# Performance work log

Hardware: AMD Instinct MI355X
Metric: run time of the kernel (lower is better)

Reference implementation:

```python
import jax, jax.numpy as jnp
import numpy as np

N_NODES = 100000
N_EDGES = 3200000
D_FEAT = 128
HIDDEN = 64
N_GRAPHS = 64


def gcn_conv(x, W, b, src, dst, deg_inv_sqrt):
    # PyG GCNConv: h = D^-1/2 (A+I) D^-1/2 (x @ W) + b, with self-loops.
    h = x @ W  # [N, out]
    coeff = deg_inv_sqrt[src] * deg_inv_sqrt[dst]  # [E]
    agg = jax.ops.segment_sum(coeff[:, None] * h[src], dst, num_segments=N_NODES)
    # self-loop contribution: deg^-1 * h
    agg = agg + (deg_inv_sqrt * deg_inv_sqrt)[:, None] * h
    return agg + b


def setup_inputs() -> dict:
    key = jax.random.key(0)
    ks = jax.random.split(key, 16)
    x = jax.random.normal(ks[0], (N_NODES, D_FEAT), dtype=jnp.float32)
    edge_index = jax.random.randint(ks[1], (2, N_EDGES), 0, N_NODES, dtype=jnp.int64)
    batch = jnp.sort(jax.random.randint(ks[2], (N_NODES,), 0, N_GRAPHS, dtype=jnp.int64))
    sc_in = 1.0 / np.sqrt(D_FEAT)
    sc_h = 1.0 / np.sqrt(HIDDEN)
    return {
        "x": x,
        "edge_index": edge_index,
        "batch": batch,
        "W1": jax.random.uniform(ks[3], (D_FEAT, HIDDEN), jnp.float32, -sc_in, sc_in),
        "b1": jnp.zeros((HIDDEN,), jnp.float32),
        "mlpW": jax.random.uniform(ks[4], (HIDDEN, HIDDEN), jnp.float32, -sc_h, sc_h),
        "mlpb": jax.random.uniform(ks[5], (HIDDEN,), jnp.float32, -sc_h, sc_h),
        "W2": jax.random.uniform(ks[6], (HIDDEN, HIDDEN), jnp.float32, -sc_h, sc_h),
        "b2": jnp.zeros((HIDDEN,), jnp.float32),
        "W3": jax.random.uniform(ks[7], (HIDDEN, HIDDEN), jnp.float32, -sc_h, sc_h),
        "b3": jnp.zeros((HIDDEN,), jnp.float32),
        "linW": jax.random.uniform(ks[8], (HIDDEN, 1), jnp.float32, -sc_h, sc_h),
        "linb": jax.random.uniform(ks[9], (1,), jnp.float32, -sc_h, sc_h),
    }


def reference(x, edge_index, batch, W1, b1, mlpW, mlpb, W2, b2, W3, b3, linW, linb):
    src, dst = edge_index[0], edge_index[1]
    # symmetric gcn_norm degrees (with self-loop), computed once from dst
    deg = jax.ops.segment_sum(jnp.ones((N_EDGES,), x.dtype), dst, num_segments=N_NODES) + 1.0
    deg_inv_sqrt = jax.lax.rsqrt(deg)

    h = jax.nn.relu(gcn_conv(x, W1, b1, src, dst, deg_inv_sqrt))
    h = jax.nn.relu(h @ mlpW + mlpb)  # mlp1 (Linear); edge_index arg in source is a no-op
    h = jax.nn.relu(gcn_conv(h, W2, b2, src, dst, deg_inv_sqrt))
    h = jax.nn.relu(gcn_conv(h, W3, b3, src, dst, deg_inv_sqrt))

    # global_mean_pool over graphs
    sums = jax.ops.segment_sum(h, batch, num_segments=N_GRAPHS)  # [G, H]
    counts = jax.ops.segment_sum(jnp.ones((N_NODES,), h.dtype), batch, num_segments=N_GRAPHS)
    pooled = sums / jnp.maximum(counts, 1.0)[:, None]

    # dropout p=0.5 is identity in eval mode
    return pooled @ linW + linb  # [G, 1]
```

## Files before the change

### kernel.cpp

```cpp
#include <hip/hip_runtime.h>

#define NN 100000
#define NE 3200000
#define DF 128
#define NH 64
#define NG 64

#define BKN 256
#define NB2 ((NN + BKN - 1) / BKN)
#define CAP2 8832
#define PART_E 8192
#define PART_T 512
#define PART_NBLK ((NE + PART_E - 1) / PART_E)
#define ELLW 64

typedef _Float16 h16;
typedef unsigned char f8;
typedef __fp16 hv2 __attribute__((ext_vector_type(2)));
typedef __fp16 hv4 __attribute__((ext_vector_type(4)));
typedef float fv4 __attribute__((ext_vector_type(4)));

#define FSCALE 16.0f
#define INV_FSCALE 0.0625f

__device__ __forceinline__ f8 to_f8(float v) {
    int pk = __builtin_amdgcn_cvt_pk_fp8_f32(v, v, 0, false);
    return (f8)(pk & 0xFF);
}

__device__ __forceinline__ float dot2h(unsigned a, unsigned b, float c) {
    return __builtin_amdgcn_fdot2(__builtin_bit_cast(hv2, a),
                                  __builtin_bit_cast(hv2, b), c, false);
}

__device__ __forceinline__ unsigned pack_pair(float v) {
    int nb = __builtin_amdgcn_mov_dpp(__builtin_bit_cast(int, v), 0xB1, 0xF, 0xF, true);
    return __builtin_bit_cast(unsigned,
        __builtin_amdgcn_cvt_pkrtz(v, __builtin_bit_cast(float, nb)));
}

__device__ __forceinline__ unsigned pack_rtn(float a, float b) {
    unsigned ua = (unsigned)__builtin_bit_cast(unsigned short, (h16)a);
    unsigned ub = (unsigned)__builtin_bit_cast(unsigned short, (h16)b);
    return ua | (ub << 16);
}


__global__ void k_init(int* __restrict__ bcur) {
    int i = threadIdx.x;
    if (i < NB2) bcur[i] = i * CAP2;
}


__global__ __launch_bounds__(PART_T) void k_part(const int* __restrict__ src,
                                                 const int* __restrict__ dst,
                                                 int* __restrict__ bcur,
                                                 int* __restrict__ tmp) {
    __shared__ int ds[PART_E];
    __shared__ int hist[NB2];
    __shared__ int base[NB2];
    int t = threadIdx.x;
    int e0 = blockIdx.x * PART_E;
    int ne = NE - e0; if (ne > PART_E) ne = PART_E;

    for (int b = t; b < NB2; b += PART_T) hist[b] = 0;
    __syncthreads();
    for (int i = t; i < ne; i += PART_T) {
        int d = dst[e0 + i];
        ds[i] = d;
        atomicAdd(&hist[d >> 8], 1);
    }
    __syncthreads();
    for (int b = t; b < NB2; b += PART_T)
        base[b] = atomicAdd(&bcur[b], hist[b]);
    __syncthreads();
    for (int i = t; i < ne; i += PART_T) {
        int d = ds[i];
        int s = src[e0 + i];
        int pos = atomicAdd(&base[d >> 8], 1);
        tmp[pos] = (s << 8) | (d & (BKN - 1));
    }
}


__global__ __launch_bounds__(256) void k_build(const int* __restrict__ bcur,
                                               const int* __restrict__ tmp,
                                               float* __restrict__ dis,
                                               int* __restrict__ cnt,
                                               int* __restrict__ csr,
                                               float* __restrict__ sums,
                                               f8* __restrict__ A,
                                               f8* __restrict__ B) {
    __shared__ int h[BKN];
    __shared__ int cur[BKN];
    int b = blockIdx.x, t = threadIdx.x;
    if (b == 0) { for (int i = t; i < NG * NH + NG; i += 256) sums[i] = 0.f; }
    if (b == 1 && t < NH) {
        A[(size_t)NN * NH + t] = 0;
        B[(size_t)NN * NH + t] = 0;
    }
    h[t] = 0;
    __syncthreads();
    int beg = b * CAP2, end = bcur[b];
    for (int i = beg + t; i < end; i += 256) atomicAdd(&h[tmp[i] & (BKN - 1)], 1);
    __syncthreads();
    int node = b * BKN + t;
    int real = h[t];
    int rmax = h[t & ~1] > h[t | 1] ? h[t & ~1] : h[t | 1];
    int common = (rmax + 3) & ~3;
    if (node < NN) {
        dis[node] = rsqrtf((float)real + 1.0f);
        cnt[node] = common;
    }
    cur[t] = 0;
    __syncthreads();
    for (int i = beg + t; i < end; i += 256) {
        int e = tmp[i];
        int d = e & (BKN - 1);
        int j = atomicAdd(&cur[d], 1);
        int nd = b * BKN + d;
        int pos = ((nd >> 1) << 7) + ((j >> 2) << 3) + ((nd & 1) << 2) + (j & 3);
        csr[pos] = (e >> 8) << 6;
    }
    __syncthreads();
    if (node < NN) {
        int pbase = (node >> 1) << 7;
        int half = (node & 1) << 2;
        for (int j = real; j < common; j++)
            csr[pbase + ((j >> 2) << 3) + half + (j & 3)] = NN << 6;
    }
}


__global__ __launch_bounds__(256) void k_gemm1(const float* __restrict__ x,
                                               const float* __restrict__ W1,
                                               const float* __restrict__ dis,
                                               f8* __restrict__ out) {
    int t = threadIdx.x;
    int lane = t & 63;
    int tile = blockIdx.x * 4 + (t >> 6);
    if (tile >= NN / 16) return;
    int r16 = lane & 15, g4 = lane >> 4;

    hv4 b[4][8];
#pragma unroll
    for (int s = 0; s < 8; s++) {
#pragma unroll
        for (int ct = 0; ct < 4; ct++) {
            const float* wp = W1 + (s * 16 + g4 * 4) * NH + ct * 16 + r16;
            hv4 bb;
            bb[0] = (h16)wp[0];
            bb[1] = (h16)wp[NH];
            bb[2] = (h16)wp[2 * NH];
            bb[3] = (h16)wp[3 * NH];
            b[ct][s] = bb;
        }
    }

    int nb = tile * 16;
    const float* xw = x + (size_t)(nb + r16) * DF + g4 * 4;
    fv4 xr[8];
#pragma unroll
    for (int s = 0; s < 8; s++) xr[s] = *(const fv4*)(xw + s * 16);

    fv4 acc[4] = {fv4{0.f, 0.f, 0.f, 0.f}, fv4{0.f, 0.f, 0.f, 0.f},
                  fv4{0.f, 0.f, 0.f, 0.f}, fv4{0.f, 0.f, 0.f, 0.f}};
#pragma unroll
    for (int s = 0; s < 8; s++) {
        hv4 a;
        a[0] = (h16)xr[s][0]; a[1] = (h16)xr[s][1];
        a[2] = (h16)xr[s][2]; a[3] = (h16)xr[s][3];
#pragma unroll
        for (int ct = 0; ct < 4; ct++)
            acc[ct] = __builtin_amdgcn_mfma_f32_16x16x16f16(a, b[ct][s], acc[ct], 0, 0, 0);
    }

    float dv[4];
#pragma unroll
    for (int r = 0; r < 4; r++) dv[r] = dis[nb + g4 * 4 + r] * FSCALE;
#pragma unroll
    for (int ct = 0; ct < 4; ct++) {
#pragma unroll
        for (int r = 0; r < 4; r++) {
            int n = nb + g4 * 4 + r;
            out[((unsigned)n << 6) | (unsigned)(ct * 16 + r16)] = to_f8(dv[r] * acc[ct][r]);
        }
    }
}


__device__ __forceinline__ float f8_ld(const f8* __restrict__ hs, unsigned off) {
    return __builtin_amdgcn_cvt_f32_fp8((int)hs[off], 0);
}

#define ACC8(qa, qb)                                                    \
    do {                                                                \
        a0 += f8_ld(hs, ((unsigned)(qa).x) | lane);                     \
        a1 += f8_ld(hs, ((unsigned)(qa).y) | lane);                     \
        a0 += f8_ld(hs, ((unsigned)(qa).z) | lane);                     \
        a1 += f8_ld(hs, ((unsigned)(qa).w) | lane);                     \
        b0 += f8_ld(hs, ((unsigned)(qb).x) | lane);                     \
        b1 += f8_ld(hs, ((unsigned)(qb).y) | lane);                     \
        b0 += f8_ld(hs, ((unsigned)(qb).z) | lane);                     \
        b1 += f8_ld(hs, ((unsigned)(qb).w) | lane);                     \
    } while (0)

__device__ __forceinline__ void gather_pair(const int* __restrict__ csr,
                                            const int* __restrict__ cnt,
                                            const f8* __restrict__ hs,
                                            int p, unsigned lane,
                                            float& g0, float& g1) {
    int beg = __builtin_amdgcn_readfirstlane(p << 7);
    int len = __builtin_amdgcn_readfirstlane(cnt[2 * p]);
    int end = beg + 2 * len;
    float a0 = f8_ld(hs, ((unsigned)(2 * p) << 6) | lane);
    float b0 = f8_ld(hs, ((unsigned)(2 * p + 1) << 6) | lane);
    float a1 = 0.f, b1 = 0.f;
    int k = beg;
    if (k + 16 <= end) {
        int4 qa = *(const int4*)(csr + k);
        int4 qb = *(const int4*)(csr + k + 4);
        int4 qc = *(const int4*)(csr + k + 8);
        int4 qd = *(const int4*)(csr + k + 12);
        for (; k + 32 <= end; k += 16) {
            int4 na = *(const int4*)(csr + k + 16);
            int4 nb = *(const int4*)(csr + k + 20);
            int4 nc = *(const int4*)(csr + k + 24);
            int4 nd = *(const int4*)(csr + k + 28);
            ACC8(qa, qb);
            ACC8(qc, qd);
            qa = na; qb = nb; qc = nc; qd = nd;
        }
        ACC8(qa, qb);
        ACC8(qc, qd);
        k += 16;
    }
    if (k + 8 <= end) {
        int4 qa = *(const int4*)(csr + k);
        int4 qb = *(const int4*)(csr + k + 4);
        ACC8(qa, qb);
    }
    g0 = a0 + a1;
    g1 = b0 + b1;
}


__global__ __launch_bounds__(1024) void k_gather_mm2(const int* __restrict__ cnt,
                                                     const int* __restrict__ csr,
                                                     const float* __restrict__ dis,
                                                     const f8* __restrict__ hs,
                                                     const float* __restrict__ bin,
                                                     const float* __restrict__ W1m,
                                                     const float* __restrict__ bmid,
                                                     const float* __restrict__ W2m,
                                                     f8* __restrict__ outp) {
    __shared__ unsigned w1p[(NH / 2) * NH];
    __shared__ unsigned w2p[(NH / 2) * NH];
    __shared__ unsigned pvl[16][2][NH / 2];
    __shared__ float b_in[NH], b_mid[NH];
    int t = threadIdx.x;
    for (int i = t; i < (NH / 2) * NH; i += 1024) {
        int k2 = i >> 6, o = i & 63;
        w1p[i] = pack_rtn(W1m[(2 * k2) * NH + o], W1m[(2 * k2 + 1) * NH + o]);
        w2p[i] = pack_rtn(W2m[(2 * k2) * NH + o], W2m[(2 * k2 + 1) * NH + o]);
    }
    if (t < NH) { b_in[t] = bin[t]; b_mid[t] = bmid[t]; }
    __syncthreads();

    int wave = t >> 6, lane = t & 63;
    int p = blockIdx.x * 16 + wave;
    int n0 = 2 * p, n1 = 2 * p + 1;
    float d0 = dis[n0], d1 = dis[n1];

    float g0, g1;
    gather_pair(csr, cnt, hs, p, (unsigned)lane, g0, g1);
    float v0 = fmaxf(g0 * (d0 * INV_FSCALE) + b_in[lane], 0.f);
    float v1 = fmaxf(g1 * (d1 * INV_FSCALE) + b_in[lane], 0.f);

    unsigned pv0 = pack_pair(v0), pv1 = pack_pair(v1);
    if (!(lane & 1)) {
        pvl[wave][0][lane >> 1] = pv0;
        pvl[wave][1][lane >> 1] = pv1;
    }
    float m0 = 0.f, m1 = 0.f;
#pragma unroll
    for (int k4 = 0; k4 < 8; k4++) {
        int4 a0 = *(const int4*)&pvl[wave][0][k4 * 4];
        int4 a1 = *(const int4*)&pvl[wave][1][k4 * 4];
        unsigned wv;
        wv = w1p[(k4 * 4 + 0) * NH + lane]; m0 = dot2h((unsigned)a0.x, wv, m0); m1 = dot2h((unsigned)a1.x, wv, m1);
        wv = w1p[(k4 * 4 + 1) * NH + lane]; m0 = dot2h((unsigned)a0.y, wv, m0); m1 = dot2h((unsigned)a1.y, wv, m1);
        wv = w1p[(k4 * 4 + 2) * NH + lane]; m0 = dot2h((unsigned)a0.z, wv, m0); m1 = dot2h((unsigned)a1.z, wv, m1);
        wv = w1p[(k4 * 4 + 3) * NH + lane]; m0 = dot2h((unsigned)a0.w, wv, m0); m1 = dot2h((unsigned)a1.w, wv, m1);
    }
    m0 = fmaxf(m0 + b_mid[lane], 0.f);
    m1 = fmaxf(m1 + b_mid[lane], 0.f);

    unsigned pm0 = pack_pair(m0), pm1 = pack_pair(m1);
    if (!(lane & 1)) {
        pvl[wave][0][lane >> 1] = pm0;
        pvl[wave][1][lane >> 1] = pm1;
    }
    float o0 = 0.f, o1 = 0.f;
#pragma unroll
    for (int k4 = 0; k4 < 8; k4++) {
        int4 a0 = *(const int4*)&pvl[wave][0][k4 * 4];
        int4 a1 = *(const int4*)&pvl[wave][1][k4 * 4];
        unsigned wv;
        wv = w2p[(k4 * 4 + 0) * NH + lane]; o0 = dot2h((unsigned)a0.x, wv, o0); o1 = dot2h((unsigned)a1.x, wv, o1);
        wv = w2p[(k4 * 4 + 1) * NH + lane]; o0 = dot2h((unsigned)a0.y, wv, o0); o1 = dot2h((unsigned)a1.y, wv, o1);
        wv = w2p[(k4 * 4 + 2) * NH + lane]; o0 = dot2h((unsigned)a0.z, wv, o0); o1 = dot2h((unsigned)a1.z, wv, o1);
        wv = w2p[(k4 * 4 + 3) * NH + lane]; o0 = dot2h((unsigned)a0.w, wv, o0); o1 = dot2h((unsigned)a1.w, wv, o1);
    }
    outp[((unsigned)n0 << 6) | (unsigned)lane] = to_f8(d0 * o0 * FSCALE);
    outp[((unsigned)n1 << 6) | (unsigned)lane] = to_f8(d1 * o1 * FSCALE);
}


__global__ __launch_bounds__(1024) void k_gather_mm1(const int* __restrict__ cnt,
                                                     const int* __restrict__ csr,
                                                     const float* __restrict__ dis,
                                                     const f8* __restrict__ hs,
                                                     const float* __restrict__ bin,
                                                     const float* __restrict__ W1m,
                                                     f8* __restrict__ outp) {
    __shared__ unsigned w1p[(NH / 2) * NH];
    __shared__ unsigned pvl[16][2][NH / 2];
    __shared__ float b_in[NH];
    int t = threadIdx.x;
    for (int i = t; i < (NH / 2) * NH; i += 1024) {
        int k2 = i >> 6, o = i & 63;
        w1p[i] = pack_rtn(W1m[(2 * k2) * NH + o], W1m[(2 * k2 + 1) * NH + o]);
    }
    if (t < NH) b_in[t] = bin[t];
    __syncthreads();

    int wave = t >> 6, lane = t & 63;
    int p = blockIdx.x * 16 + wave;
    int n0 = 2 * p, n1 = 2 * p + 1;
    float d0 = dis[n0], d1 = dis[n1];

    float g0, g1;
    gather_pair(csr, cnt, hs, p, (unsigned)lane, g0, g1);
    float v0 = fmaxf(g0 * (d0 * INV_FSCALE) + b_in[lane], 0.f);
    float v1 = fmaxf(g1 * (d1 * INV_FSCALE) + b_in[lane], 0.f);

    unsigned pv0 = pack_pair(v0), pv1 = pack_pair(v1);
    if (!(lane & 1)) {
        pvl[wave][0][lane >> 1] = pv0;
        pvl[wave][1][lane >> 1] = pv1;
    }
    float o0 = 0.f, o1 = 0.f;
#pragma unroll
    for (int k4 = 0; k4 < 8; k4++) {
        int4 a0 = *(const int4*)&pvl[wave][0][k4 * 4];
        int4 a1 = *(const int4*)&pvl[wave][1][k4 * 4];
        unsigned wv;
        wv = w1p[(k4 * 4 + 0) * NH + lane]; o0 = dot2h((unsigned)a0.x, wv, o0); o1 = dot2h((unsigned)a1.x, wv, o1);
        wv = w1p[(k4 * 4 + 1) * NH + lane]; o0 = dot2h((unsigned)a0.y, wv, o0); o1 = dot2h((unsigned)a1.y, wv, o1);
        wv = w1p[(k4 * 4 + 2) * NH + lane]; o0 = dot2h((unsigned)a0.z, wv, o0); o1 = dot2h((unsigned)a1.z, wv, o1);
        wv = w1p[(k4 * 4 + 3) * NH + lane]; o0 = dot2h((unsigned)a0.w, wv, o0); o1 = dot2h((unsigned)a1.w, wv, o1);
    }
    outp[((unsigned)n0 << 6) | (unsigned)lane] = to_f8(d0 * o0 * FSCALE);
    outp[((unsigned)n1 << 6) | (unsigned)lane] = to_f8(d1 * o1 * FSCALE);
}


__global__ __launch_bounds__(1024) void k_gather_pool(const int* __restrict__ cnt,
                                                      const int* __restrict__ csr,
                                                      const float* __restrict__ dis,
                                                      const f8* __restrict__ hs,
                                                      const float* __restrict__ b3,
                                                      const int* __restrict__ batch,
                                                      float* __restrict__ sums,
                                                      float* __restrict__ cntf) {
    __shared__ float rows[32][NH];
    __shared__ int gids[32];
    int t = threadIdx.x;
    int wave = t >> 6, lane = t & 63;
    int p = blockIdx.x * 16 + wave;
    int n0 = 2 * p, n1 = 2 * p + 1;
    {
        float d0 = dis[n0], d1 = dis[n1];
        float g0, g1;
        gather_pair(csr, cnt, hs, p, (unsigned)lane, g0, g1);
        rows[2 * wave][lane]     = fmaxf(g0 * (d0 * INV_FSCALE) + b3[lane], 0.f);
        rows[2 * wave + 1][lane] = fmaxf(g1 * (d1 * INV_FSCALE) + b3[lane], 0.f);
        if (lane == 0) { gids[2 * wave] = batch[n0]; gids[2 * wave + 1] = batch[n1]; }
    }
    __syncthreads();
    if (wave == 0) {
        float acc = 0.f; float cl = 0.f;
        int cur = gids[0];
        for (int i = 0; i < 32; i++) {
            int g = gids[i];
            if (g != cur) {
                atomicAdd(&sums[cur * NH + lane], acc);
                if (lane == 0) atomicAdd(&cntf[cur], cl);
                acc = 0.f; cl = 0.f; cur = g;
            }
            acc += rows[i][lane];
            cl += 1.f;
        }
        atomicAdd(&sums[cur * NH + lane], acc);
        if (lane == 0) atomicAdd(&cntf[cur], cl);
    }
}


__global__ void k_final(const float* __restrict__ sums, const float* __restrict__ cnt,
                        const float* __restrict__ linW, const float* __restrict__ linb,
                        float* __restrict__ out) {
    int g = blockIdx.x;
    int lane = threadIdx.x;
    float v = sums[g * NH + lane] * linW[lane];
#pragma unroll
    for (int off = 32; off > 0; off >>= 1) v += __shfl_down(v, off);
    if (lane == 0) out[g] = v / fmaxf(cnt[g], 1.f) + linb[0];
}


extern "C" void kernel_launch(void* const* d_in, const int* in_sizes, int n_in,
                              void* d_out, int out_size, void* d_ws, size_t ws_size,
                              hipStream_t stream) {
    const float* x    = (const float*)d_in[0];
    const int*   ei   = (const int*)d_in[1];
    const int*   batch= (const int*)d_in[2];
    const float* W1   = (const float*)d_in[3];
    const float* b1   = (const float*)d_in[4];
    const float* mlpW = (const float*)d_in[5];
    const float* mlpb = (const float*)d_in[6];
    const float* W2   = (const float*)d_in[7];
    const float* b2   = (const float*)d_in[8];
    const float* W3   = (const float*)d_in[9];
    const float* b3   = (const float*)d_in[10];
    const float* linW = (const float*)d_in[11];
    const float* linb = (const float*)d_in[12];
    float* out = (float*)d_out;

    char* p = (char*)d_ws;
    int*   csr  = (int*)p;                p += (size_t)NN * ELLW * 4;
    f8*    A    = (f8*)p;                 p += (size_t)(NN + 1) * NH;
    f8*    B    = (f8*)p;                 p += (size_t)(NN + 1) * NH;
    int*   tmp  = (int*)p;                p += (size_t)NB2 * CAP2 * 4;
    float* dis  = (float*)p;              p += NN * 4;
    float* sums = (float*)p;              p += NG * NH * 4;
    float* cntf = (float*)p;              p += NG * 4;
    int*   cnt  = (int*)p;                p += NN * 4;
    int*   bcur = (int*)p;                p += 512 * 4;

    const int* src = ei;
    const int* dst = ei + NE;

    k_init<<<1, 512, 0, stream>>>(bcur);
    k_part<<<PART_NBLK, PART_T, 0, stream>>>(src, dst, bcur, tmp);
    k_build<<<NB2, 256, 0, stream>>>(bcur, tmp, dis, cnt, csr, sums, A, B);

    k_gemm1<<<(NN / 16 + 3) / 4, 256, 0, stream>>>(x, W1, dis, A);
    k_gather_mm2<<<NN / 32, 1024, 0, stream>>>(cnt, csr, dis, A, b1, mlpW, mlpb, W2, B);

    k_gather_mm1<<<NN / 32, 1024, 0, stream>>>(cnt, csr, dis, B, b2, W3, A);

    k_gather_pool<<<NN / 32, 1024, 0, stream>>>(cnt, csr, dis, A, b3, batch, sums, cntf);

    k_final<<<NG, 64, 0, stream>>>(sums, cntf, linW, linb, out);
}
```

Baseline: 347.9 us.

## Process four nodes per wave with interleaved dual-pair gather

Each wave now handles two node pairs (four nodes) instead of one pair. The two neighbor-list gathers are interleaved in one loop to expose more independent memory loads, and each weight value read from LDS is reused across four rows in the dense mini-GEMMs. The grid shrinks by half and out-of-range waves exit early. In exchange each wave uses more registers, which may cut occupancy, and the second pair's tail is handled serially when its degree differs from the first pair's.

New measurement: 351.4 us. About the same (+1.0%).

```diff
diff --git a/kernel.cpp b/kernel.cpp
--- a/kernel.cpp
+++ b/kernel.cpp
@@ -13,6 +13,8 @@
 #define PART_T 512
 #define PART_NBLK ((NE + PART_E - 1) / PART_E)
 #define ELLW 64
+#define NQUAD 25000
+#define GRID_G ((NQUAD + 15) / 16)
 
 typedef _Float16 h16;
 typedef unsigned char f8;
@@ -193,55 +195,61 @@
     return __builtin_amdgcn_cvt_f32_fp8((int)hs[off], 0);
 }
 
-#define ACC8(qa, qb)                                                    \
+#define ACC8G(qa, qb, A0, A1, B0, B1)                                   \
     do {                                                                \
-        a0 += f8_ld(hs, ((unsigned)(qa).x) | lane);                     \
-        a1 += f8_ld(hs, ((unsigned)(qa).y) | lane);                     \
-        a0 += f8_ld(hs, ((unsigned)(qa).z) | lane);                     \
-        a1 += f8_ld(hs, ((unsigned)(qa).w) | lane);                     \
-        b0 += f8_ld(hs, ((unsigned)(qb).x) | lane);                     \
-        b1 += f8_ld(hs, ((unsigned)(qb).y) | lane);                     \
-        b0 += f8_ld(hs, ((unsigned)(qb).z) | lane);                     \
-        b1 += f8_ld(hs, ((unsigned)(qb).w) | lane);                     \
+        A0 += f8_ld(hs, ((unsigned)(qa).x) | lane);                     \
+        A1 += f8_ld(hs, ((unsigned)(qa).y) | lane);                     \
+        A0 += f8_ld(hs, ((unsigned)(qa).z) | lane);                     \
+        A1 += f8_ld(hs, ((unsigned)(qa).w) | lane);                     \
+        B0 += f8_ld(hs, ((unsigned)(qb).x) | lane);                     \
+        B1 += f8_ld(hs, ((unsigned)(qb).y) | lane);                     \
+        B0 += f8_ld(hs, ((unsigned)(qb).z) | lane);                     \
+        B1 += f8_ld(hs, ((unsigned)(qb).w) | lane);                     \
     } while (0)
 
-__device__ __forceinline__ void gather_pair(const int* __restrict__ csr,
+__device__ __forceinline__ void gather_dual(const int* __restrict__ csr,
                                             const int* __restrict__ cnt,
                                             const f8* __restrict__ hs,
-                                            int p, unsigned lane,
-                                            float& g0, float& g1) {
-    int beg = __builtin_amdgcn_readfirstlane(p << 7);
-    int len = __builtin_amdgcn_readfirstlane(cnt[2 * p]);
-    int end = beg + 2 * len;
-    float a0 = f8_ld(hs, ((unsigned)(2 * p) << 6) | lane);
-    float b0 = f8_ld(hs, ((unsigned)(2 * p + 1) << 6) | lane);
-    float a1 = 0.f, b1 = 0.f;
-    int k = beg;
-    if (k + 16 <= end) {
-        int4 qa = *(const int4*)(csr + k);
-        int4 qb = *(const int4*)(csr + k + 4);
-        int4 qc = *(const int4*)(csr + k + 8);
-        int4 qd = *(const int4*)(csr + k + 12);
-        for (; k + 32 <= end; k += 16) {
-            int4 na = *(const int4*)(csr + k + 16);
-            int4 nb = *(const int4*)(csr + k + 20);
-            int4 nc = *(const int4*)(csr + k + 24);
-            int4 nd = *(const int4*)(csr + k + 28);
-            ACC8(qa, qb);
-            ACC8(qc, qd);
-            qa = na; qb = nb; qc = nc; qd = nd;
-        }
-        ACC8(qa, qb);
-        ACC8(qc, qd);
-        k += 16;
-    }
-    if (k + 8 <= end) {
-        int4 qa = *(const int4*)(csr + k);
-        int4 qb = *(const int4*)(csr + k + 4);
-        ACC8(qa, qb);
-    }
-    g0 = a0 + a1;
-    g1 = b0 + b1;
+                                            int q, unsigned lane,
+                                            float& g0, float& g1,
+                                            float& g2, float& g3) {
+    int pA = 2 * q, pB = 2 * q + 1;
+    int begA = __builtin_amdgcn_readfirstlane(pA << 7);
+    int lenA = __builtin_amdgcn_readfirstlane(cnt[2 * pA]);
+    int endA = begA + 2 * lenA;
+    int begB = __builtin_amdgcn_readfirstlane(pB << 7);
+    int lenB = __builtin_amdgcn_readfirstlane(cnt[2 * pB]);
+    int endB = begB + 2 * lenB;
+
+    float a0 = f8_ld(hs, ((unsigned)(2 * pA) << 6) | lane);
+    float b0 = f8_ld(hs, ((unsigned)(2 * pA + 1) << 6) | lane);
+    float c0 = f8_ld(hs, ((unsigned)(2 * pB) << 6) | lane);
+    float d0 = f8_ld(hs, ((unsigned)(2 * pB + 1) << 6) | lane);
+    float a1 = 0.f, b1 = 0.f, c1 = 0.f, d1 = 0.f;
+
+    int kA = begA, kB = begB;
+    int4 qaA = *(const int4*)(csr + kA), qbA = *(const int4*)(csr + kA + 4);
+    int4 qaB = *(const int4*)(csr + kB), qbB = *(const int4*)(csr + kB + 4);
+
+    while (kA + 16 <= endA && kB + 16 <= endB) {
+        int4 naA = *(const int4*)(csr + kA + 8),  nbA = *(const int4*)(csr + kA + 12);
+        int4 naB = *(const int4*)(csr + kB + 8),  nbB = *(const int4*)(csr + kB + 12);
+        ACC8G(qaA, qbA, a0, a1, b0, b1);
+        ACC8G(qaB, qbB, c0, c1, d0, d1);
+        qaA = naA; qbA = nbA; qaB = naB; qbB = nbB;
+        kA += 8; kB += 8;
+    }
+    ACC8G(qaA, qbA, a0, a1, b0, b1); kA += 8;
+    ACC8G(qaB, qbB, c0, c1, d0, d1); kB += 8;
+    for (; kA + 8 <= endA; kA += 8) {
+        int4 qa = *(const int4*)(csr + kA), qb = *(const int4*)(csr + kA + 4);
+        ACC8G(qa, qb, a0, a1, b0, b1);
+    }
+    for (; kB + 8 <= endB; kB += 8) {
+        int4 qa = *(const int4*)(csr + kB), qb = *(const int4*)(csr + kB + 4);
+        ACC8G(qa, qb, c0, c1, d0, d1);
+    }
+    g0 = a0 + a1; g1 = b0 + b1; g2 = c0 + c1; g3 = d0 + d1;
 }
 
 
@@ -256,7 +264,7 @@
                                                      f8* __restrict__ outp) {
     __shared__ unsigned w1p[(NH / 2) * NH];
     __shared__ unsigned w2p[(NH / 2) * NH];
-    __shared__ unsigned pvl[16][2][NH / 2];
+    __shared__ unsigned pvl[16][4][NH / 2];
     __shared__ float b_in[NH], b_mid[NH];
     int t = threadIdx.x;
     for (int i = t; i < (NH / 2) * NH; i += 1024) {
@@ -268,52 +276,82 @@
     __syncthreads();
 
     int wave = t >> 6, lane = t & 63;
-    int p = blockIdx.x * 16 + wave;
-    int n0 = 2 * p, n1 = 2 * p + 1;
-    float d0 = dis[n0], d1 = dis[n1];
-
-    float g0, g1;
-    gather_pair(csr, cnt, hs, p, (unsigned)lane, g0, g1);
-    float v0 = fmaxf(g0 * (d0 * INV_FSCALE) + b_in[lane], 0.f);
-    float v1 = fmaxf(g1 * (d1 * INV_FSCALE) + b_in[lane], 0.f);
-
-    unsigned pv0 = pack_pair(v0), pv1 = pack_pair(v1);
+    int q = blockIdx.x * 16 + wave;
+    if (q >= NQUAD) return;
+    int n0 = 4 * q;
+    float dd[4];
+#pragma unroll
+    for (int i = 0; i < 4; i++) dd[i] = dis[n0 + i];
+
+    float g[4];
+    gather_dual(csr, cnt, hs, q, (unsigned)lane, g[0], g[1], g[2], g[3]);
+    float m[4], o[4];
+    unsigned pv[4];
+#pragma unroll
+    for (int i = 0; i < 4; i++) {
+        float v = fmaxf(g[i] * (dd[i] * INV_FSCALE) + b_in[lane], 0.f);
+        pv[i] = pack_pair(v);
+    }
     if (!(lane & 1)) {
-        pvl[wave][0][lane >> 1] = pv0;
-        pvl[wave][1][lane >> 1] = pv1;
-    }
-    float m0 = 0.f, m1 = 0.f;
+#pragma unroll
+        for (int i = 0; i < 4; i++) pvl[wave][i][lane >> 1] = pv[i];
+    }
+#pragma unroll
+    for (int i = 0; i < 4; i++) m[i] = 0.f;
 #pragma unroll
     for (int k4 = 0; k4 < 8; k4++) {
         int4 a0 = *(const int4*)&pvl[wave][0][k4 * 4];
         int4 a1 = *(const int4*)&pvl[wave][1][k4 * 4];
+        int4 a2 = *(const int4*)&pvl[wave][2][k4 * 4];
+        int4 a3 = *(const int4*)&pvl[wave][3][k4 * 4];
         unsigned wv;
-        wv = w1p[(k4 * 4 + 0) * NH + lane]; m0 = dot2h((unsigned)a0.x, wv, m0); m1 = dot2h((unsigned)a1.x, wv, m1);
-        wv = w1p[(k4 * 4 + 1) * NH + lane]; m0 = dot2h((unsigned)a0.y, wv, m0); m1 = dot2h((unsigned)a1.y, wv, m1);
-        wv = w1p[(k4 * 4 + 2) * NH + lane]; m0 = dot2h((unsigned)a0.z, wv, m0); m1 = dot2h((unsigned)a1.z, wv, m1);
-        wv = w1p[(k4 * 4 + 3) * NH + lane]; m0 = dot2h((unsigned)a0.w, wv, m0); m1 = dot2h((unsigned)a1.w, wv, m1);
-    }
-    m0 = fmaxf(m0 + b_mid[lane], 0.f);
-    m1 = fmaxf(m1 + b_mid[lane], 0.f);
-
-    unsigned pm0 = pack_pair(m0), pm1 = pack_pair(m1);
+        wv = w1p[(k4 * 4 + 0) * NH + lane];
+        m[0] = dot2h((unsigned)a0.x, wv, m[0]); m[1] = dot2h((unsigned)a1.x, wv, m[1]);
+        m[2] = dot2h((unsigned)a2.x, wv, m[2]); m[3] = dot2h((unsigned)a3.x, wv, m[3]);
+        wv = w1p[(k4 * 4 + 1) * NH + lane];
+        m[0] = dot2h((unsigned)a0.y, wv, m[0]); m[1] = dot2h((unsigned)a1.y, wv, m[1]);
+        m[2] = dot2h((unsigned)a2.y, wv, m[2]); m[3] = dot2h((unsigned)a3.y, wv, m[3]);
+        wv = w1p[(k4 * 4 + 2) * NH + lane];
+        m[0] = dot2h((unsigned)a0.z, wv, m[0]); m[1] = dot2h((unsigned)a1.z, wv, m[1]);
+        m[2] = dot2h((unsigned)a2.z, wv, m[2]); m[3] = dot2h((unsigned)a3.z, wv, m[3]);
+        wv = w1p[(k4 * 4 + 3) * NH + lane];
+        m[0] = dot2h((unsigned)a0.w, wv, m[0]); m[1] = dot2h((unsigned)a1.w, wv, m[1]);
+        m[2] = dot2h((unsigned)a2.w, wv, m[2]); m[3] = dot2h((unsigned)a3.w, wv, m[3]);
+    }
+#pragma unroll
+    for (int i = 0; i < 4; i++) {
+        m[i] = fmaxf(m[i] + b_mid[lane], 0.f);
+        pv[i] = pack_pair(m[i]);
+    }
     if (!(lane & 1)) {
-        pvl[wave][0][lane >> 1] = pm0;
-        pvl[wave][1][lane >> 1] = pm1;
-    }
-    float o0 = 0.f, o1 = 0.f;
+#pragma unroll
+        for (int i = 0; i < 4; i++) pvl[wave][i][lane >> 1] = pv[i];
+    }
+#pragma unroll
+    for (int i = 0; i < 4; i++) o[i] = 0.f;
 #pragma unroll
     for (int k4 = 0; k4 < 8; k4++) {
         int4 a0 = *(const int4*)&pvl[wave][0][k4 * 4];
         int4 a1 = *(const int4*)&pvl[wave][1][k4 * 4];
+        int4 a2 = *(const int4*)&pvl[wave][2][k4 * 4];
+        int4 a3 = *(const int4*)&pvl[wave][3][k4 * 4];
         unsigned wv;
-        wv = w2p[(k4 * 4 + 0) * NH + lane]; o0 = dot2h((unsigned)a0.x, wv, o0); o1 = dot2h((unsigned)a1.x, wv, o1);
-        wv = w2p[(k4 * 4 + 1) * NH + lane]; o0 = dot2h((unsigned)a0.y, wv, o0); o1 = dot2h((unsigned)a1.y, wv, o1);
-        wv = w2p[(k4 * 4 + 2) * NH + lane]; o0 = dot2h((unsigned)a0.z, wv, o0); o1 = dot2h((unsigned)a1.z, wv, o1);
-        wv = w2p[(k4 * 4 + 3) * NH + lane]; o0 = dot2h((unsigned)a0.w, wv, o0); o1 = dot2h((unsigned)a1.w, wv, o1);
-    }
-    outp[((unsigned)n0 << 6) | (unsigned)lane] = to_f8(d0 * o0 * FSCALE);
-    outp[((unsigned)n1 << 6) | (unsigned)lane] = to_f8(d1 * o1 * FSCALE);
+        wv = w2p[(k4 * 4 + 0) * NH + lane];
+        o[0] = dot2h((unsigned)a0.x, wv, o[0]); o[1] = dot2h((unsigned)a1.x, wv, o[1]);
+        o[2] = dot2h((unsigned)a2.x, wv, o[2]); o[3] = dot2h((unsigned)a3.x, wv, o[3]);
+        wv = w2p[(k4 * 4 + 1) * NH + lane];
+        o[0] = dot2h((unsigned)a0.y, wv, o[0]); o[1] = dot2h((unsigned)a1.y, wv, o[1]);
+        o[2] = dot2h((unsigned)a2.y, wv, o[2]); o[3] = dot2h((unsigned)a3.y, wv, o[3]);
+        wv = w2p[(k4 * 4 + 2) * NH + lane];
+        o[0] = dot2h((unsigned)a0.z, wv, o[0]); o[1] = dot2h((unsigned)a1.z, wv, o[1]);
+        o[2] = dot2h((unsigned)a2.z, wv, o[2]); o[3] = dot2h((unsigned)a3.z, wv, o[3]);
+        wv = w2p[(k4 * 4 + 3) * NH + lane];
+        o[0] = dot2h((unsigned)a0.w, wv, o[0]); o[1] = dot2h((unsigned)a1.w, wv, o[1]);
+        o[2] = dot2h((unsigned)a2.w, wv, o[2]); o[3] = dot2h((unsigned)a3.w, wv, o[3]);
+    }
+#pragma unroll
+    for (int i = 0; i < 4; i++)
+        outp[((unsigned)(n0 + i) << 6) | (unsigned)lane] = to_f8(dd[i] * o[i] * FSCALE);
 }
 
 
@@ -325,7 +363,7 @@
                                                      const float* __restrict__ W1m,
                                                      f8* __restrict__ outp) {
     __shared__ unsigned w1p[(NH / 2) * NH];
-    __shared__ unsigned pvl[16][2][NH / 2];
+    __shared__ unsigned pvl[16][4][NH / 2];
     __shared__ float b_in[NH];
     int t = threadIdx.x;
     for (int i = t; i < (NH / 2) * NH; i += 1024) {
@@ -336,33 +374,50 @@
     __syncthreads();
 
     int wave = t >> 6, lane = t & 63;
-    int p = blockIdx.x * 16 + wave;
-    int n0 = 2 * p, n1 = 2 * p + 1;
-    float d0 = dis[n0], d1 = dis[n1];
-
-    float g0, g1;
-    gather_pair(csr, cnt, hs, p, (unsigned)lane, g0, g1);
-    float v0 = fmaxf(g0 * (d0 * INV_FSCALE) + b_in[lane], 0.f);
-    float v1 = fmaxf(g1 * (d1 * INV_FSCALE) + b_in[lane], 0.f);
-
-    unsigned pv0 = pack_pair(v0), pv1 = pack_pair(v1);
+    int q = blockIdx.x * 16 + wave;
+    if (q >= NQUAD) return;
+    int n0 = 4 * q;
+    float dd[4];
+#pragma unroll
+    for (int i = 0; i < 4; i++) dd[i] = dis[n0 + i];
+
+    float g[4], o[4];
+    unsigned pv[4];
+    gather_dual(csr, cnt, hs, q, (unsigned)lane, g[0], g[1], g[2], g[3]);
+#pragma unroll
+    for (int i = 0; i < 4; i++) {
+        float v = fmaxf(g[i] * (dd[i] * INV_FSCALE) + b_in[lane], 0.f);
+        pv[i] = pack_pair(v);
+    }
     if (!(lane & 1)) {
-        pvl[wave][0][lane >> 1] = pv0;
-        pvl[wave][1][lane >> 1] = pv1;
-    }
-    float o0 = 0.f, o1 = 0.f;
+#pragma unroll
+        for (int i = 0; i < 4; i++) pvl[wave][i][lane >> 1] = pv[i];
+    }
+#pragma unroll
+    for (int i = 0; i < 4; i++) o[i] = 0.f;
 #pragma unroll
     for (int k4 = 0; k4 < 8; k4++) {
         int4 a0 = *(const int4*)&pvl[wave][0][k4 * 4];
         int4 a1 = *(const int4*)&pvl[wave][1][k4 * 4];
+        int4 a2 = *(const int4*)&pvl[wave][2][k4 * 4];
+        int4 a3 = *(const int4*)&pvl[wave][3][k4 * 4];
         unsigned wv;
-        wv = w1p[(k4 * 4 + 0) * NH + lane]; o0 = dot2h((unsigned)a0.x, wv, o0); o1 = dot2h((unsigned)a1.x, wv, o1);
-        wv = w1p[(k4 * 4 + 1) * NH + lane]; o0 = dot2h((unsigned)a0.y, wv, o0); o1 = dot2h((unsigned)a1.y, wv, o1);
-        wv = w1p[(k4 * 4 + 2) * NH + lane]; o0 = dot2h((unsigned)a0.z, wv, o0); o1 = dot2h((unsigned)a1.z, wv, o1);
-        wv = w1p[(k4 * 4 + 3) * NH + lane]; o0 = dot2h((unsigned)a0.w, wv, o0); o1 = dot2h((unsigned)a1.w, wv, o1);
-    }
-    outp[((unsigned)n0 << 6) | (unsigned)lane] = to_f8(d0 * o0 * FSCALE);
-    outp[((unsigned)n1 << 6) | (unsigned)lane] = to_f8(d1 * o1 * FSCALE);
+        wv = w1p[(k4 * 4 + 0) * NH + lane];
+        o[0] = dot2h((unsigned)a0.x, wv, o[0]); o[1] = dot2h((unsigned)a1.x, wv, o[1]);
+        o[2] = dot2h((unsigned)a2.x, wv, o[2]); o[3] = dot2h((unsigned)a3.x, wv, o[3]);
+        wv = w1p[(k4 * 4 + 1) * NH + lane];
+        o[0] = dot2h((unsigned)a0.y, wv, o[0]); o[1] = dot2h((unsigned)a1.y, wv, o[1]);
+        o[2] = dot2h((unsigned)a2.y, wv, o[2]); o[3] = dot2h((unsigned)a3.y, wv, o[3]);
+        wv = w1p[(k4 * 4 + 2) * NH + lane];
+        o[0] = dot2h((unsigned)a0.z, wv, o[0]); o[1] = dot2h((unsigned)a1.z, wv, o[1]);
+        o[2] = dot2h((unsigned)a2.z, wv, o[2]); o[3] = dot2h((unsigned)a3.z, wv, o[3]);
+        wv = w1p[(k4 * 4 + 3) * NH + lane];
+        o[0] = dot2h((unsigned)a0.w, wv, o[0]); o[1] = dot2h((unsigned)a1.w, wv, o[1]);
+        o[2] = dot2h((unsigned)a2.w, wv, o[2]); o[3] = dot2h((unsigned)a3.w, wv, o[3]);
+    }
+#pragma unroll
+    for (int i = 0; i < 4; i++)
+        outp[((unsigned)(n0 + i) << 6) | (unsigned)lane] = to_f8(dd[i] * o[i] * FSCALE);
 }
 
 
@@ -374,26 +429,36 @@
                                                       const int* __restrict__ batch,
                                                       float* __restrict__ sums,
                                                       float* __restrict__ cntf) {
-    __shared__ float rows[32][NH];
-    __shared__ int gids[32];
+    __shared__ float rows[64][NH];
+    __shared__ int gids[64];
     int t = threadIdx.x;
     int wave = t >> 6, lane = t & 63;
-    int p = blockIdx.x * 16 + wave;
-    int n0 = 2 * p, n1 = 2 * p + 1;
-    {
-        float d0 = dis[n0], d1 = dis[n1];
-        float g0, g1;
-        gather_pair(csr, cnt, hs, p, (unsigned)lane, g0, g1);
-        rows[2 * wave][lane]     = fmaxf(g0 * (d0 * INV_FSCALE) + b3[lane], 0.f);
-        rows[2 * wave + 1][lane] = fmaxf(g1 * (d1 * INV_FSCALE) + b3[lane], 0.f);
-        if (lane == 0) { gids[2 * wave] = batch[n0]; gids[2 * wave + 1] = batch[n1]; }
+    int q = blockIdx.x * 16 + wave;
+    bool act = q < NQUAD;
+    if (act) {
+        int n0 = 4 * q;
+        float g[4];
+        gather_dual(csr, cnt, hs, q, (unsigned)lane, g[0], g[1], g[2], g[3]);
+#pragma unroll
+        for (int i = 0; i < 4; i++) {
+            float d = dis[n0 + i];
+            rows[4 * wave + i][lane] = fmaxf(g[i] * (d * INV_FSCALE) + b3[lane], 0.f);
+        }
+        if (lane == 0) {
+#pragma unroll
+            for (int i = 0; i < 4; i++) gids[4 * wave + i] = batch[n0 + i];
+        }
+    } else if (lane == 0) {
+#pragma unroll
+        for (int i = 0; i < 4; i++) gids[4 * wave + i] = -1;
     }
     __syncthreads();
     if (wave == 0) {
         float acc = 0.f; float cl = 0.f;
         int cur = gids[0];
-        for (int i = 0; i < 32; i++) {
+        for (int i = 0; i < 64; i++) {
             int g = gids[i];
+            if (g < 0) break;
             if (g != cur) {
                 atomicAdd(&sums[cur * NH + lane], acc);
                 if (lane == 0) atomicAdd(&cntf[cur], cl);
@@ -457,11 +522,11 @@
     k_build<<<NB2, 256, 0, stream>>>(bcur, tmp, dis, cnt, csr, sums, A, B);
 
     k_gemm1<<<(NN / 16 + 3) / 4, 256, 0, stream>>>(x, W1, dis, A);
-    k_gather_mm2<<<NN / 32, 1024, 0, stream>>>(cnt, csr, dis, A, b1, mlpW, mlpb, W2, B);
-
-    k_gather_mm1<<<NN / 32, 1024, 0, stream>>>(cnt, csr, dis, B, b2, W3, A);
-
-    k_gather_pool<<<NN / 32, 1024, 0, stream>>>(cnt, csr, dis, A, b3, batch, sums, cntf);
+    k_gather_mm2<<<GRID_G, 1024, 0, stream>>>(cnt, csr, dis, A, b1, mlpW, mlpb, W2, B);
+
+    k_gather_mm1<<<GRID_G, 1024, 0, stream>>>(cnt, csr, dis, B, b2, W3, A);
+
+    k_gather_pool<<<GRID_G, 1024, 0, stream>>>(cnt, csr, dis, A, b3, batch, sums, cntf);
 
     k_final<<<NG, 64, 0, stream>>>(sums, cntf, linW, linb, out);
 }
```
